# Kernel tuning notes

Hardware: AMD Instinct MI355X
Metric: run time of the kernel (lower is better)

Reference implementation:

```python
import jax, jax.numpy as jnp
import numpy as np
import math

DIM, HEADS = 512, 8
D_K = DIM // HEADS

def setup_inputs() -> dict:
    key = jax.random.key(0)
    ks = jax.random.split(key, 6)
    B, LK, LQ = 16, 2048, 256
    s = 1.0 / math.sqrt(DIM)
    return {
        "L": jax.random.normal(ks[0], (B, LK, DIM), jnp.float32),
        "G": jax.random.normal(ks[1], (B, LQ, DIM), jnp.float32),
        "Wq": jax.random.normal(ks[2], (DIM, DIM), jnp.float32) * s,
        "bq": jnp.zeros((DIM,), jnp.float32),
        "Wo": jax.random.normal(ks[3], (DIM, DIM), jnp.float32) * s,
        "bo": jnp.zeros((DIM,), jnp.float32),
    }

def reference(L, G, Wq, bq, Wo, bo):
    B = G.shape[0]
    # Q projection from global tokens; K,V are raw local features split into heads
    q = (G @ Wq + bq).reshape(B, -1, HEADS, D_K)          # [B, Lq, H, d]
    k = L.reshape(B, -1, HEADS, D_K)                      # [B, Lk, H, d]
    v = k
    # double scaling as in source: / sqrt(d_k) * dim**-0.5
    scale = (D_K ** -0.5) * (DIM ** -0.5)
    dots = jnp.einsum("bqhd,bkhd->bhqk", q, k) * scale    # [B, H, Lq, Lk]
    attn = jax.nn.softmax(dots, axis=-1)
    x = jnp.einsum("bhqk,bkhd->bqhd", attn, v)            # [B, Lq, H, d]
    x = x.reshape(B, -1, HEADS * D_K)
    return x @ Wo + bo
```

## Files before the change

kernel.cpp:

```cpp
#include <hip/hip_runtime.h>

#define KSTR 72

typedef __attribute__((ext_vector_type(8))) short short8;
typedef __attribute__((ext_vector_type(4))) float f32x4;

#define EXP2F(x) __builtin_amdgcn_exp2f(x)

__device__ __forceinline__ unsigned short f2bf(float f) {
    union { float f; unsigned u; } v; v.f = f;
    unsigned r = v.u + 0x7fff + ((v.u >> 16) & 1);
    return (unsigned short)(r >> 16);
}
__device__ __forceinline__ unsigned pk2(float a, float b) {
    return (unsigned)f2bf(a) | ((unsigned)f2bf(b) << 16);
}

template<bool A_BF16, bool OUT_BF16>
__global__ __launch_bounds__(256) void gemm_mfma(const void* __restrict__ Ap,
                                                 const float* __restrict__ W,
                                                 const float* __restrict__ bias,
                                                 void* __restrict__ Cp,
                                                 float oscale) {
    __shared__ unsigned short As [64 * 40];
    __shared__ unsigned short Bst[64 * 40];

    const int tid  = threadIdx.x;
    const int wv   = tid >> 6;
    const int lane = tid & 63;
    const int c    = lane & 15;
    const int quad = lane >> 4;
    const int m0 = blockIdx.x * 64, n0 = blockIdx.y * 64;

    f32x4 acc[4];
    #pragma unroll
    for (int nt = 0; nt < 4; nt++) acc[nt] = (f32x4){0.f, 0.f, 0.f, 0.f};

    for (int k0 = 0; k0 < 512; k0 += 32) {
        {
            int m = tid >> 2, q8 = tid & 3;
            if (A_BF16) {
                const unsigned short* A = (const unsigned short*)Ap;
                short8 v = *(const short8*)(A + (size_t)(m0 + m) * 512 + k0 + 8 * q8);
                *(short8*)&As[m * 40 + 8 * q8] = v;
            } else {
                const float* A = (const float*)Ap;
                const float* ap = A + (size_t)(m0 + m) * 512 + k0 + 8 * q8;
                float4 a0 = *(const float4*)ap;
                float4 a1 = *(const float4*)(ap + 4);
                uint4 u;
                u.x = pk2(a0.x, a0.y); u.y = pk2(a0.z, a0.w);
                u.z = pk2(a1.x, a1.y); u.w = pk2(a1.z, a1.w);
                *(uint4*)&As[m * 40 + 8 * q8] = u;
            }
        }
        {
            int n = tid & 63, kw = tid >> 6;
            const float* wp = W + (size_t)(k0 + 8 * kw) * 512 + n0 + n;
            float bv[8];
            #pragma unroll
            for (int i = 0; i < 8; i++) bv[i] = wp[(size_t)i * 512];
            uint4 u;
            u.x = pk2(bv[0], bv[1]); u.y = pk2(bv[2], bv[3]);
            u.z = pk2(bv[4], bv[5]); u.w = pk2(bv[6], bv[7]);
            *(uint4*)&Bst[n * 40 + 8 * kw] = u;
        }
        __syncthreads();
        short8 af = *(const short8*)&As[(16 * wv + c) * 40 + 8 * quad];
        #pragma unroll
        for (int nt = 0; nt < 4; nt++) {
            short8 bf = *(const short8*)&Bst[(16 * nt + c) * 40 + 8 * quad];
            acc[nt] = __builtin_amdgcn_mfma_f32_16x16x32_bf16(af, bf, acc[nt], 0, 0, 0);
        }
        __syncthreads();
    }

    #pragma unroll
    for (int nt = 0; nt < 4; nt++) {
        float bv = bias[n0 + 16 * nt + c];
        #pragma unroll
        for (int r = 0; r < 4; r++) {
            float v = (acc[nt][r] + bv) * oscale;
            size_t idx = (size_t)(m0 + 16 * wv + 4 * quad + r) * 512 + n0 + 16 * nt + c;
            if (OUT_BF16) ((unsigned short*)Cp)[idx] = f2bf(v);
            else          ((float*)Cp)[idx] = v;
        }
    }
}

__global__ __launch_bounds__(256) void attn_mfma(const unsigned short* __restrict__ Q,
                                                 const float* __restrict__ Lmat,
                                                 unsigned short* __restrict__ X) {
    __shared__ unsigned short Krm[2][64 * KSTR];
    __shared__ unsigned short Kt [2][64 * KSTR];
    __shared__ unsigned short Pw [4][16 * KSTR];

    const int blk  = blockIdx.x;
    const int qt   = blk & 3;
    const int h    = (blk >> 2) & 7;
    const int b    = blk >> 5;
    const int tid  = threadIdx.x;
    const int wv   = tid >> 6;
    const int lane = tid & 63;
    const int c    = lane & 15;
    const int quad = lane >> 4;

    short8 qa[2];
    {
        const unsigned short* qsrc =
            Q + ((size_t)(b * 256 + qt * 64 + 16 * wv + c)) * 512 + h * 64;
        qa[0] = *(const short8*)(qsrc + 8 * quad);
        qa[1] = *(const short8*)(qsrc + 32 + 8 * quad);
    }
    short8 ones;
    #pragma unroll
    for (int i = 0; i < 8; i++) ones[i] = (short)0x3F80;

    f32x4 oacc[4];
    #pragma unroll
    for (int dt = 0; dt < 4; dt++) oacc[dt] = (f32x4){0.f, 0.f, 0.f, 0.f};
    f32x4 lacc = (f32x4){0.f, 0.f, 0.f, 0.f};

    const float* sp0 = Lmat + (size_t)b * 2048 * 512 + h * 64 + (size_t)lane * 512 + 16 * wv;

    {
        float4 a0 = *(const float4*)sp0;
        float4 a1 = *(const float4*)(sp0 + 4);
        float4 a2 = *(const float4*)(sp0 + 8);
        float4 a3 = *(const float4*)(sp0 + 12);
        uint4 u0, u1;
        u0.x = pk2(a0.x, a0.y); u0.y = pk2(a0.z, a0.w);
        u0.z = pk2(a1.x, a1.y); u0.w = pk2(a1.z, a1.w);
        u1.x = pk2(a2.x, a2.y); u1.y = pk2(a2.z, a2.w);
        u1.z = pk2(a3.x, a3.y); u1.w = pk2(a3.z, a3.w);
        *(uint4*)&Krm[0][lane * KSTR + 16 * wv]     = u0;
        *(uint4*)&Krm[0][lane * KSTR + 16 * wv + 8] = u1;
        float vals[16] = {a0.x, a0.y, a0.z, a0.w, a1.x, a1.y, a1.z, a1.w,
                          a2.x, a2.y, a2.z, a2.w, a3.x, a3.y, a3.z, a3.w};
        #pragma unroll
        for (int i = 0; i < 16; i++)
            Kt[0][(16 * wv + i) * KSTR + lane] = f2bf(vals[i]);
    }
    __syncthreads();

    const int swc = (c >> 3) & 1;
    const int swr = (quad >> 1) & 1;

    int p = 0;
    for (int t = 0; t < 32; t++) {
        float4 a0, a1, a2, a3;
        if (t < 31) {
            const float* src = sp0 + (size_t)(t + 1) * 64 * 512;
            a0 = *(const float4*)src;
            a1 = *(const float4*)(src + 4);
            a2 = *(const float4*)(src + 8);
            a3 = *(const float4*)(src + 12);
        }

        f32x4 sacc[4];
        #pragma unroll
        for (int nt = 0; nt < 4; nt++) sacc[nt] = (f32x4){0.f, 0.f, 0.f, 0.f};
        #pragma unroll
        for (int nt = 0; nt < 4; nt++)
            #pragma unroll
            for (int ks = 0; ks < 2; ks++) {
                short8 kb = *(const short8*)&Krm[p][(16 * nt + c) * KSTR + 32 * ks + 8 * quad];
                sacc[nt] = __builtin_amdgcn_mfma_f32_16x16x32_bf16(qa[ks], kb, sacc[nt], 0, 0, 0);
            }

        #pragma unroll
        for (int nt = 0; nt < 4; nt++)
            #pragma unroll
            for (int r = 0; r < 4; r++)
                Pw[wv][(4 * quad + r) * KSTR + ((16 * nt + c) ^ (8 * swr))] =
                    f2bf(EXP2F(sacc[nt][r]));

        short8 pa0 = *(const short8*)&Pw[wv][c * KSTR + (8 * (quad ^ swc))];
        short8 pa1 = *(const short8*)&Pw[wv][c * KSTR + 32 + (8 * (quad ^ swc))];

        #pragma unroll
        for (int dt = 0; dt < 4; dt++) {
            short8 v0 = *(const short8*)&Kt[p][(16 * dt + c) * KSTR + 8 * quad];
            oacc[dt] = __builtin_amdgcn_mfma_f32_16x16x32_bf16(pa0, v0, oacc[dt], 0, 0, 0);
            short8 v1 = *(const short8*)&Kt[p][(16 * dt + c) * KSTR + 32 + 8 * quad];
            oacc[dt] = __builtin_amdgcn_mfma_f32_16x16x32_bf16(pa1, v1, oacc[dt], 0, 0, 0);
        }
        lacc = __builtin_amdgcn_mfma_f32_16x16x32_bf16(pa0, ones, lacc, 0, 0, 0);
        lacc = __builtin_amdgcn_mfma_f32_16x16x32_bf16(pa1, ones, lacc, 0, 0, 0);

        if (t < 31) {
            uint4 u0, u1;
            u0.x = pk2(a0.x, a0.y); u0.y = pk2(a0.z, a0.w);
            u0.z = pk2(a1.x, a1.y); u0.w = pk2(a1.z, a1.w);
            u1.x = pk2(a2.x, a2.y); u1.y = pk2(a2.z, a2.w);
            u1.z = pk2(a3.x, a3.y); u1.w = pk2(a3.z, a3.w);
            *(uint4*)&Krm[p ^ 1][lane * KSTR + 16 * wv]     = u0;
            *(uint4*)&Krm[p ^ 1][lane * KSTR + 16 * wv + 8] = u1;
            float vals[16] = {a0.x, a0.y, a0.z, a0.w, a1.x, a1.y, a1.z, a1.w,
                              a2.x, a2.y, a2.z, a2.w, a3.x, a3.y, a3.z, a3.w};
            #pragma unroll
            for (int i = 0; i < 16; i++)
                Kt[p ^ 1][(16 * wv + i) * KSTR + lane] = f2bf(vals[i]);
        }
        __syncthreads();
        p ^= 1;
    }

    #pragma unroll
    for (int r = 0; r < 4; r++) {
        float inv = 1.f / lacc[r];
        size_t row = (size_t)(b * 256 + qt * 64 + 16 * wv + 4 * quad + r);
        unsigned short* xp = X + row * 512 + h * 64;
        #pragma unroll
        for (int dt = 0; dt < 4; dt++)
            xp[16 * dt + c] = f2bf(oacc[dt][r] * inv);
    }
}

extern "C" void kernel_launch(void* const* d_in, const int* in_sizes, int n_in,
                              void* d_out, int out_size, void* d_ws, size_t ws_size,
                              hipStream_t stream) {
    const float* Lmat = (const float*)d_in[0];
    const float* G    = (const float*)d_in[1];
    const float* Wq   = (const float*)d_in[2];
    const float* bq   = (const float*)d_in[3];
    const float* Wo   = (const float*)d_in[4];
    const float* bo   = (const float*)d_in[5];
    float* out = (float*)d_out;

    unsigned short* Qws = (unsigned short*)d_ws;
    unsigned short* Xws = Qws + (size_t)4096 * 512;

    const float SCe = 0.005524271728019903f * 1.4426950408889634f;

    dim3 gg(64, 8);
    gemm_mfma<false, true><<<gg, 256, 0, stream>>>(G, Wq, bq, Qws, SCe);
    attn_mfma<<<512, 256, 0, stream>>>(Qws, Lmat, Xws);
    gemm_mfma<true, false><<<gg, 256, 0, stream>>>(Xws, Wo, bo, out, 1.0f);
}
```

Measured before the change: 200.8 us.

## Pre-convert L and weights into MFMA fragment layout in workspace

```diff
diff --git a/kernel.cpp b/kernel.cpp
--- a/kernel.cpp
+++ b/kernel.cpp
@@ -14,6 +14,226 @@
 }
 __device__ __forceinline__ unsigned pk2(float a, float b) {
     return (unsigned)f2bf(a) | ((unsigned)f2bf(b) << 16);
+}
+
+
+__global__ __launch_bounds__(256) void conv_W(const float* __restrict__ Wq,
+                                              const float* __restrict__ Wo,
+                                              unsigned short* __restrict__ WqF,
+                                              unsigned short* __restrict__ WoF) {
+    const float* W = blockIdx.y ? Wo : Wq;
+    unsigned short* WF = blockIdx.y ? WoF : WqF;
+    int g = blockIdx.x * 256 + threadIdx.x;
+    int lane = g & 63, ntg = (g >> 6) & 31, kt = g >> 11;
+    int c = lane & 15, quad = lane >> 4;
+    const float* wp = W + (size_t)(32 * kt + 8 * quad) * 512 + 16 * ntg + c;
+    float v[8];
+    #pragma unroll
+    for (int j = 0; j < 8; j++) v[j] = wp[(size_t)j * 512];
+    uint4 u;
+    u.x = pk2(v[0], v[1]); u.y = pk2(v[2], v[3]);
+    u.z = pk2(v[4], v[5]); u.w = pk2(v[6], v[7]);
+    *(uint4*)(WF + (size_t)g * 8) = u;
+}
+
+__global__ __launch_bounds__(256) void conv_L(const float* __restrict__ Lmat,
+                                              unsigned short* __restrict__ KF,
+                                              unsigned short* __restrict__ VF) {
+    __shared__ unsigned short KFs[4096];
+    __shared__ unsigned short VFs[4096];
+    const int blk = blockIdx.x;
+    const int t = blk & 31, h = (blk >> 5) & 7, b = blk >> 8;
+    const int tid = threadIdx.x;
+    const int key = tid & 63, wv = tid >> 6;
+
+    const float* src = Lmat + ((size_t)(b * 2048 + 64 * t + key)) * 512 + 64 * h + 16 * wv;
+    float4 a0 = *(const float4*)src;
+    float4 a1 = *(const float4*)(src + 4);
+    float4 a2 = *(const float4*)(src + 8);
+    float4 a3 = *(const float4*)(src + 12);
+    float vals[16] = {a0.x, a0.y, a0.z, a0.w, a1.x, a1.y, a1.z, a1.w,
+                      a2.x, a2.y, a2.z, a2.w, a3.x, a3.y, a3.z, a3.w};
+    #pragma unroll
+    for (int i = 0; i < 16; i++) {
+        int d = 16 * wv + i;
+        unsigned short bv = f2bf(vals[i]);
+        KFs[((((key >> 4) * 2 + (d >> 5)) * 64) + ((d >> 3) & 3) * 16 + (key & 15)) * 8 + (d & 7)] = bv;
+        VFs[((((d >> 4) * 2 + (key >> 5)) * 64) + ((key >> 3) & 3) * 16 + (d & 15)) * 8 + (key & 7)] = bv;
+    }
+    __syncthreads();
+    size_t gbase = (size_t)blk * 4096 + tid * 16;
+    *(uint4*)(KF + gbase)     = *(const uint4*)&KFs[tid * 16];
+    *(uint4*)(KF + gbase + 8) = *(const uint4*)&KFs[tid * 16 + 8];
+    *(uint4*)(VF + gbase)     = *(const uint4*)&VFs[tid * 16];
+    *(uint4*)(VF + gbase + 8) = *(const uint4*)&VFs[tid * 16 + 8];
+}
+
+template<bool A_BF16, bool OUT_BF16>
+__global__ __launch_bounds__(256) void gemm_frag(const void* __restrict__ Ap,
+                                                 const unsigned short* __restrict__ WF,
+                                                 const float* __restrict__ bias,
+                                                 void* __restrict__ Cp,
+                                                 float oscale) {
+    __shared__ unsigned short As[64 * 72];
+    const int tid = threadIdx.x;
+    const int wv = tid >> 6, lane = tid & 63;
+    const int c = lane & 15, quad = lane >> 4;
+    const int m0 = blockIdx.x * 64, n0 = blockIdx.y * 64;
+
+    f32x4 acc[4];
+    #pragma unroll
+    for (int nt = 0; nt < 4; nt++) acc[nt] = (f32x4){0.f, 0.f, 0.f, 0.f};
+
+    for (int k0 = 0; k0 < 512; k0 += 64) {
+        {
+            int m = tid >> 2, seg = tid & 3;
+            if (A_BF16) {
+                const unsigned short* ap = (const unsigned short*)Ap +
+                    (size_t)(m0 + m) * 512 + k0 + 16 * seg;
+                *(uint4*)&As[m * 72 + 16 * seg]     = *(const uint4*)ap;
+                *(uint4*)&As[m * 72 + 16 * seg + 8] = *(const uint4*)(ap + 8);
+            } else {
+                const float* ap = (const float*)Ap + (size_t)(m0 + m) * 512 + k0 + 16 * seg;
+                float4 b0 = *(const float4*)ap;
+                float4 b1 = *(const float4*)(ap + 4);
+                float4 b2 = *(const float4*)(ap + 8);
+                float4 b3 = *(const float4*)(ap + 12);
+                uint4 u0, u1;
+                u0.x = pk2(b0.x, b0.y); u0.y = pk2(b0.z, b0.w);
+                u0.z = pk2(b1.x, b1.y); u0.w = pk2(b1.z, b1.w);
+                u1.x = pk2(b2.x, b2.y); u1.y = pk2(b2.z, b2.w);
+                u1.z = pk2(b3.x, b3.y); u1.w = pk2(b3.z, b3.w);
+                *(uint4*)&As[m * 72 + 16 * seg]     = u0;
+                *(uint4*)&As[m * 72 + 16 * seg + 8] = u1;
+            }
+        }
+        __syncthreads();
+        #pragma unroll
+        for (int kk = 0; kk < 2; kk++) {
+            short8 af = *(const short8*)&As[(16 * wv + c) * 72 + 32 * kk + 8 * quad];
+            #pragma unroll
+            for (int nt = 0; nt < 4; nt++) {
+                short8 bf = *(const short8*)(WF +
+                    (((size_t)(k0 / 32 + kk) * 32 + n0 / 16 + nt) * 64 + lane) * 8);
+                acc[nt] = __builtin_amdgcn_mfma_f32_16x16x32_bf16(af, bf, acc[nt], 0, 0, 0);
+            }
+        }
+        __syncthreads();
+    }
+
+    #pragma unroll
+    for (int nt = 0; nt < 4; nt++) {
+        float bv = bias[n0 + 16 * nt + c];
+        #pragma unroll
+        for (int r = 0; r < 4; r++) {
+            float v = (acc[nt][r] + bv) * oscale;
+            size_t idx = (size_t)(m0 + 16 * wv + 4 * quad + r) * 512 + n0 + 16 * nt + c;
+            if (OUT_BF16) ((unsigned short*)Cp)[idx] = f2bf(v);
+            else          ((float*)Cp)[idx] = v;
+        }
+    }
+}
+
+__global__ __launch_bounds__(256) void attn_frag(const unsigned short* __restrict__ Q,
+                                                 const unsigned short* __restrict__ KF,
+                                                 const unsigned short* __restrict__ VF,
+                                                 unsigned short* __restrict__ X) {
+    __shared__ unsigned short Pw[4][16 * KSTR];
+
+    const int blk = blockIdx.x;
+    const int qt = blk & 3, h = (blk >> 2) & 7, b = blk >> 5;
+    const int tid = threadIdx.x;
+    const int wv = tid >> 6, lane = tid & 63;
+    const int c = lane & 15, quad = lane >> 4;
+
+    short8 qa[2];
+    {
+        const unsigned short* qsrc =
+            Q + ((size_t)(b * 256 + qt * 64 + 16 * wv + c)) * 512 + h * 64;
+        qa[0] = *(const short8*)(qsrc + 8 * quad);
+        qa[1] = *(const short8*)(qsrc + 32 + 8 * quad);
+    }
+    short8 ones;
+    #pragma unroll
+    for (int i = 0; i < 8; i++) ones[i] = (short)0x3F80;
+
+    f32x4 oacc[4];
+    #pragma unroll
+    for (int dt = 0; dt < 4; dt++) oacc[dt] = (f32x4){0.f, 0.f, 0.f, 0.f};
+    f32x4 lacc = (f32x4){0.f, 0.f, 0.f, 0.f};
+
+    const int swc = (c >> 3) & 1;
+    const int swr = (quad >> 1) & 1;
+
+    const unsigned short* kf = KF + ((size_t)((b * 8 + h) * 32)) * 4096 + lane * 8;
+    const unsigned short* vf = VF + ((size_t)((b * 8 + h) * 32)) * 4096 + lane * 8;
+
+    short8 kc[8], vc[8], kn[8], vn[8];
+    #pragma unroll
+    for (int f = 0; f < 8; f++) {
+        kc[f] = *(const short8*)(kf + f * 512);
+        vc[f] = *(const short8*)(vf + f * 512);
+    }
+
+    auto compute = [&](short8* kb, short8* vb) {
+        f32x4 sacc[4];
+        #pragma unroll
+        for (int nt = 0; nt < 4; nt++) sacc[nt] = (f32x4){0.f, 0.f, 0.f, 0.f};
+        #pragma unroll
+        for (int nt = 0; nt < 4; nt++)
+            #pragma unroll
+            for (int ks = 0; ks < 2; ks++)
+                sacc[nt] = __builtin_amdgcn_mfma_f32_16x16x32_bf16(
+                    qa[ks], kb[nt * 2 + ks], sacc[nt], 0, 0, 0);
+        #pragma unroll
+        for (int nt = 0; nt < 4; nt++)
+            #pragma unroll
+            for (int r = 0; r < 4; r++)
+                Pw[wv][(4 * quad + r) * KSTR + ((16 * nt + c) ^ (8 * swr))] =
+                    f2bf(EXP2F(sacc[nt][r]));
+        short8 pa0 = *(const short8*)&Pw[wv][c * KSTR + (8 * (quad ^ swc))];
+        short8 pa1 = *(const short8*)&Pw[wv][c * KSTR + 32 + (8 * (quad ^ swc))];
+        #pragma unroll
+        for (int dt = 0; dt < 4; dt++) {
+            oacc[dt] = __builtin_amdgcn_mfma_f32_16x16x32_bf16(pa0, vb[dt * 2], oacc[dt], 0, 0, 0);
+            oacc[dt] = __builtin_amdgcn_mfma_f32_16x16x32_bf16(pa1, vb[dt * 2 + 1], oacc[dt], 0, 0, 0);
+        }
+        lacc = __builtin_amdgcn_mfma_f32_16x16x32_bf16(pa0, ones, lacc, 0, 0, 0);
+        lacc = __builtin_amdgcn_mfma_f32_16x16x32_bf16(pa1, ones, lacc, 0, 0, 0);
+    };
+
+    for (int t = 0; t < 32; t += 2) {
+        {
+            const unsigned short* k2 = kf + (size_t)(t + 1) * 4096;
+            const unsigned short* v2 = vf + (size_t)(t + 1) * 4096;
+            #pragma unroll
+            for (int f = 0; f < 8; f++) {
+                kn[f] = *(const short8*)(k2 + f * 512);
+                vn[f] = *(const short8*)(v2 + f * 512);
+            }
+        }
+        compute(kc, vc);
+        if (t + 2 < 32) {
+            const unsigned short* k2 = kf + (size_t)(t + 2) * 4096;
+            const unsigned short* v2 = vf + (size_t)(t + 2) * 4096;
+            #pragma unroll
+            for (int f = 0; f < 8; f++) {
+                kc[f] = *(const short8*)(k2 + f * 512);
+                vc[f] = *(const short8*)(v2 + f * 512);
+            }
+        }
+        compute(kn, vn);
+    }
+
+    #pragma unroll
+    for (int r = 0; r < 4; r++) {
+        float inv = 1.f / lacc[r];
+        size_t row = (size_t)(b * 256 + qt * 64 + 16 * wv + 4 * quad + r);
+        unsigned short* xp = X + row * 512 + h * 64;
+        #pragma unroll
+        for (int dt = 0; dt < 4; dt++)
+            xp[16 * dt + c] = f2bf(oacc[dt][r] * inv);
+    }
 }
 
 template<bool A_BF16, bool OUT_BF16>
@@ -24,18 +244,15 @@
                                                  float oscale) {
     __shared__ unsigned short As [64 * 40];
     __shared__ unsigned short Bst[64 * 40];
-
     const int tid  = threadIdx.x;
     const int wv   = tid >> 6;
     const int lane = tid & 63;
     const int c    = lane & 15;
     const int quad = lane >> 4;
     const int m0 = blockIdx.x * 64, n0 = blockIdx.y * 64;
-
     f32x4 acc[4];
     #pragma unroll
     for (int nt = 0; nt < 4; nt++) acc[nt] = (f32x4){0.f, 0.f, 0.f, 0.f};
-
     for (int k0 = 0; k0 < 512; k0 += 32) {
         {
             int m = tid >> 2, q8 = tid & 3;
@@ -74,7 +291,6 @@
         }
         __syncthreads();
     }
-
     #pragma unroll
     for (int nt = 0; nt < 4; nt++) {
         float bv = bias[n0 + 16 * nt + c];
@@ -94,7 +310,6 @@
     __shared__ unsigned short Krm[2][64 * KSTR];
     __shared__ unsigned short Kt [2][64 * KSTR];
     __shared__ unsigned short Pw [4][16 * KSTR];
-
     const int blk  = blockIdx.x;
     const int qt   = blk & 3;
     const int h    = (blk >> 2) & 7;
@@ -104,7 +319,6 @@
     const int lane = tid & 63;
     const int c    = lane & 15;
     const int quad = lane >> 4;
-
     short8 qa[2];
     {
         const unsigned short* qsrc =
@@ -115,14 +329,11 @@
     short8 ones;
     #pragma unroll
     for (int i = 0; i < 8; i++) ones[i] = (short)0x3F80;
-
     f32x4 oacc[4];
     #pragma unroll
     for (int dt = 0; dt < 4; dt++) oacc[dt] = (f32x4){0.f, 0.f, 0.f, 0.f};
     f32x4 lacc = (f32x4){0.f, 0.f, 0.f, 0.f};
-
     const float* sp0 = Lmat + (size_t)b * 2048 * 512 + h * 64 + (size_t)lane * 512 + 16 * wv;
-
     {
         float4 a0 = *(const float4*)sp0;
         float4 a1 = *(const float4*)(sp0 + 4);
@@ -142,10 +353,8 @@
             Kt[0][(16 * wv + i) * KSTR + lane] = f2bf(vals[i]);
     }
     __syncthreads();
-
     const int swc = (c >> 3) & 1;
     const int swr = (quad >> 1) & 1;
-
     int p = 0;
     for (int t = 0; t < 32; t++) {
         float4 a0, a1, a2, a3;
@@ -156,7 +365,6 @@
             a2 = *(const float4*)(src + 8);
             a3 = *(const float4*)(src + 12);
         }
-
         f32x4 sacc[4];
         #pragma unroll
         for (int nt = 0; nt < 4; nt++) sacc[nt] = (f32x4){0.f, 0.f, 0.f, 0.f};
@@ -167,17 +375,14 @@
                 short8 kb = *(const short8*)&Krm[p][(16 * nt + c) * KSTR + 32 * ks + 8 * quad];
                 sacc[nt] = __builtin_amdgcn_mfma_f32_16x16x32_bf16(qa[ks], kb, sacc[nt], 0, 0, 0);
             }
-
         #pragma unroll
         for (int nt = 0; nt < 4; nt++)
             #pragma unroll
             for (int r = 0; r < 4; r++)
                 Pw[wv][(4 * quad + r) * KSTR + ((16 * nt + c) ^ (8 * swr))] =
                     f2bf(EXP2F(sacc[nt][r]));
-
         short8 pa0 = *(const short8*)&Pw[wv][c * KSTR + (8 * (quad ^ swc))];
         short8 pa1 = *(const short8*)&Pw[wv][c * KSTR + 32 + (8 * (quad ^ swc))];
-
         #pragma unroll
         for (int dt = 0; dt < 4; dt++) {
             short8 v0 = *(const short8*)&Kt[p][(16 * dt + c) * KSTR + 8 * quad];
@@ -187,7 +392,6 @@
         }
         lacc = __builtin_amdgcn_mfma_f32_16x16x32_bf16(pa0, ones, lacc, 0, 0, 0);
         lacc = __builtin_amdgcn_mfma_f32_16x16x32_bf16(pa1, ones, lacc, 0, 0, 0);
-
         if (t < 31) {
             uint4 u0, u1;
             u0.x = pk2(a0.x, a0.y); u0.y = pk2(a0.z, a0.w);
@@ -205,7 +409,6 @@
         __syncthreads();
         p ^= 1;
     }
-
     #pragma unroll
     for (int r = 0; r < 4; r++) {
         float inv = 1.f / lacc[r];
@@ -228,13 +431,26 @@
     const float* bo   = (const float*)d_in[5];
     float* out = (float*)d_out;
 
+    const float SCe = 0.005524271728019903f * 1.4426950408889634f;
+    dim3 gg(64, 8);
+
+    const size_t NEED = 76546048;
     unsigned short* Qws = (unsigned short*)d_ws;
-    unsigned short* Xws = Qws + (size_t)4096 * 512;
-
-    const float SCe = 0.005524271728019903f * 1.4426950408889634f;
-
-    dim3 gg(64, 8);
-    gemm_mfma<false, true><<<gg, 256, 0, stream>>>(G, Wq, bq, Qws, SCe);
-    attn_mfma<<<512, 256, 0, stream>>>(Qws, Lmat, Xws);
-    gemm_mfma<true, false><<<gg, 256, 0, stream>>>(Xws, Wo, bo, out, 1.0f);
-}
+    unsigned short* Xws = Qws + (size_t)2097152;
+
+    if (ws_size >= NEED) {
+        unsigned short* WqF = Xws + (size_t)2097152;
+        unsigned short* WoF = WqF + (size_t)262144;
+        unsigned short* KF  = WoF + (size_t)262144;
+        unsigned short* VF  = KF  + (size_t)16777216;
+        conv_W<<<dim3(128, 2), 256, 0, stream>>>(Wq, Wo, WqF, WoF);
+        conv_L<<<4096, 256, 0, stream>>>(Lmat, KF, VF);
+        gemm_frag<false, true><<<gg, 256, 0, stream>>>(G, WqF, bq, Qws, SCe);
+        attn_frag<<<512, 256, 0, stream>>>(Qws, KF, VF, Xws);
+        gemm_frag<true, false><<<gg, 256, 0, stream>>>(Xws, WoF, bo, out, 1.0f);
+    } else {
+        gemm_mfma<false, true><<<gg, 256, 0, stream>>>(G, Wq, bq, Qws, SCe);
+        attn_mfma<<<512, 256, 0, stream>>>(Qws, Lmat, Xws);
+        gemm_mfma<true, false><<<gg, 256, 0, stream>>>(Xws, Wo, bo, out, 1.0f);
+    }
+}
```

After: 191.9 us. 1.05x faster.

## Pre-pack K/V and weights into MFMA fragment layout, load directly to registers

Applied to the files above, without the earlier changes.

```diff
diff --git a/kernel.cpp b/kernel.cpp
--- a/kernel.cpp
+++ b/kernel.cpp
@@ -16,63 +16,93 @@
     return (unsigned)f2bf(a) | ((unsigned)f2bf(b) << 16);
 }
 
+__global__ __launch_bounds__(256) void conv_W(const float* __restrict__ Wq,
+                                              const float* __restrict__ Wo,
+                                              unsigned short* __restrict__ WqF,
+                                              unsigned short* __restrict__ WoF) {
+    const float* W = blockIdx.y ? Wo : Wq;
+    unsigned short* WF = blockIdx.y ? WoF : WqF;
+    int g = blockIdx.x * 256 + threadIdx.x;
+    int lane = g & 63, ntg = (g >> 6) & 31, kt = g >> 11;
+    int c = lane & 15, quad = lane >> 4;
+    const float* wp = W + (size_t)(32 * kt + 8 * quad) * 512 + 16 * ntg + c;
+    float v[8];
+    #pragma unroll
+    for (int j = 0; j < 8; j++) v[j] = wp[(size_t)j * 512];
+    uint4 u;
+    u.x = pk2(v[0], v[1]); u.y = pk2(v[2], v[3]);
+    u.z = pk2(v[4], v[5]); u.w = pk2(v[6], v[7]);
+    *(uint4*)(WF + (size_t)g * 8) = u;
+}
+
+__global__ __launch_bounds__(256) void conv_L(const float* __restrict__ Lmat,
+                                              unsigned short* __restrict__ KF,
+                                              unsigned short* __restrict__ VF) {
+    __shared__ unsigned short KFs[4096];
+    __shared__ unsigned short VFs[4096];
+    const int blk = blockIdx.x;
+    const int t = blk & 31, h = (blk >> 5) & 7, b = blk >> 8;
+    const int tid = threadIdx.x;
+    const int key = tid & 63, wv = tid >> 6;
+
+    const float* src = Lmat + ((size_t)(b * 2048 + 64 * t + key)) * 512 + 64 * h + 16 * wv;
+    float4 a0 = *(const float4*)src;
+    float4 a1 = *(const float4*)(src + 4);
+    float4 a2 = *(const float4*)(src + 8);
+    float4 a3 = *(const float4*)(src + 12);
+    float vals[16] = {a0.x, a0.y, a0.z, a0.w, a1.x, a1.y, a1.z, a1.w,
+                      a2.x, a2.y, a2.z, a2.w, a3.x, a3.y, a3.z, a3.w};
+    #pragma unroll
+    for (int i = 0; i < 16; i++) {
+        int d = 16 * wv + i;
+        unsigned short bv = f2bf(vals[i]);
+        KFs[((((key >> 4) * 2 + (d >> 5)) * 64) + ((d >> 3) & 3) * 16 + (key & 15)) * 8 + (d & 7)] = bv;
+        VFs[((((d >> 4) * 2 + (key >> 5)) * 64) + ((key >> 3) & 3) * 16 + (d & 15)) * 8 + (key & 7)] = bv;
+    }
+    __syncthreads();
+    size_t gbase = (size_t)blk * 4096 + tid * 16;
+    *(uint4*)(KF + gbase)     = *(const uint4*)&KFs[tid * 16];
+    *(uint4*)(KF + gbase + 8) = *(const uint4*)&KFs[tid * 16 + 8];
+    *(uint4*)(VF + gbase)     = *(const uint4*)&VFs[tid * 16];
+    *(uint4*)(VF + gbase + 8) = *(const uint4*)&VFs[tid * 16 + 8];
+}
+
 template<bool A_BF16, bool OUT_BF16>
-__global__ __launch_bounds__(256) void gemm_mfma(const void* __restrict__ Ap,
-                                                 const float* __restrict__ W,
-                                                 const float* __restrict__ bias,
-                                                 void* __restrict__ Cp,
-                                                 float oscale) {
-    __shared__ unsigned short As [64 * 40];
-    __shared__ unsigned short Bst[64 * 40];
-
-    const int tid  = threadIdx.x;
-    const int wv   = tid >> 6;
-    const int lane = tid & 63;
-    const int c    = lane & 15;
-    const int quad = lane >> 4;
+__global__ __launch_bounds__(256) void gemm_direct(const void* __restrict__ Ap,
+                                                   const unsigned short* __restrict__ WF,
+                                                   const float* __restrict__ bias,
+                                                   void* __restrict__ Cp,
+                                                   float oscale) {
+    const int tid = threadIdx.x;
+    const int wv = tid >> 6, lane = tid & 63;
+    const int c = lane & 15, quad = lane >> 4;
     const int m0 = blockIdx.x * 64, n0 = blockIdx.y * 64;
+    const int row = m0 + 16 * wv + c;
 
     f32x4 acc[4];
     #pragma unroll
     for (int nt = 0; nt < 4; nt++) acc[nt] = (f32x4){0.f, 0.f, 0.f, 0.f};
 
-    for (int k0 = 0; k0 < 512; k0 += 32) {
-        {
-            int m = tid >> 2, q8 = tid & 3;
-            if (A_BF16) {
-                const unsigned short* A = (const unsigned short*)Ap;
-                short8 v = *(const short8*)(A + (size_t)(m0 + m) * 512 + k0 + 8 * q8);
-                *(short8*)&As[m * 40 + 8 * q8] = v;
-            } else {
-                const float* A = (const float*)Ap;
-                const float* ap = A + (size_t)(m0 + m) * 512 + k0 + 8 * q8;
-                float4 a0 = *(const float4*)ap;
-                float4 a1 = *(const float4*)(ap + 4);
-                uint4 u;
-                u.x = pk2(a0.x, a0.y); u.y = pk2(a0.z, a0.w);
-                u.z = pk2(a1.x, a1.y); u.w = pk2(a1.z, a1.w);
-                *(uint4*)&As[m * 40 + 8 * q8] = u;
-            }
-        }
-        {
-            int n = tid & 63, kw = tid >> 6;
-            const float* wp = W + (size_t)(k0 + 8 * kw) * 512 + n0 + n;
-            float bv[8];
-            #pragma unroll
-            for (int i = 0; i < 8; i++) bv[i] = wp[(size_t)i * 512];
-            uint4 u;
-            u.x = pk2(bv[0], bv[1]); u.y = pk2(bv[2], bv[3]);
-            u.z = pk2(bv[4], bv[5]); u.w = pk2(bv[6], bv[7]);
-            *(uint4*)&Bst[n * 40 + 8 * kw] = u;
-        }
-        __syncthreads();
-        short8 af = *(const short8*)&As[(16 * wv + c) * 40 + 8 * quad];
+    #pragma unroll
+    for (int kk = 0; kk < 16; kk++) {
+        short8 af;
+        if (A_BF16) {
+            af = *(const short8*)((const unsigned short*)Ap + (size_t)row * 512 + 32 * kk + 8 * quad);
+        } else {
+            const float* ap = (const float*)Ap + (size_t)row * 512 + 32 * kk + 8 * quad;
+            float4 x0 = *(const float4*)ap;
+            float4 x1 = *(const float4*)(ap + 4);
+            af[0] = (short)f2bf(x0.x); af[1] = (short)f2bf(x0.y);
+            af[2] = (short)f2bf(x0.z); af[3] = (short)f2bf(x0.w);
+            af[4] = (short)f2bf(x1.x); af[5] = (short)f2bf(x1.y);
+            af[6] = (short)f2bf(x1.z); af[7] = (short)f2bf(x1.w);
+        }
         #pragma unroll
         for (int nt = 0; nt < 4; nt++) {
-            short8 bf = *(const short8*)&Bst[(16 * nt + c) * 40 + 8 * quad];
+            short8 bf = *(const short8*)(WF +
+                (((size_t)kk * 32 + (n0 >> 4) + nt) * 64 + lane) * 8);
             acc[nt] = __builtin_amdgcn_mfma_f32_16x16x32_bf16(af, bf, acc[nt], 0, 0, 0);
         }
-        __syncthreads();
     }
 
     #pragma unroll
@@ -88,22 +118,19 @@
     }
 }
 
-__global__ __launch_bounds__(256) void attn_mfma(const unsigned short* __restrict__ Q,
-                                                 const float* __restrict__ Lmat,
+__global__ __launch_bounds__(256) void attn_frag(const unsigned short* __restrict__ Q,
+                                                 const unsigned short* __restrict__ KF,
+                                                 const unsigned short* __restrict__ VF,
                                                  unsigned short* __restrict__ X) {
-    __shared__ unsigned short Krm[2][64 * KSTR];
-    __shared__ unsigned short Kt [2][64 * KSTR];
-    __shared__ unsigned short Pw [4][16 * KSTR];
-
-    const int blk  = blockIdx.x;
-    const int qt   = blk & 3;
-    const int h    = (blk >> 2) & 7;
-    const int b    = blk >> 5;
-    const int tid  = threadIdx.x;
-    const int wv   = tid >> 6;
-    const int lane = tid & 63;
-    const int c    = lane & 15;
-    const int quad = lane >> 4;
+    __shared__ unsigned short Pw[4][16 * KSTR];
+
+    const int raw = blockIdx.x;
+    const int h  = raw & 7;
+    const int qt = (raw >> 3) & 3;
+    const int b  = raw >> 5;
+    const int tid = threadIdx.x;
+    const int wv = tid >> 6, lane = tid & 63;
+    const int c = lane & 15, quad = lane >> 4;
 
     short8 qa[2];
     {
@@ -121,89 +148,67 @@
     for (int dt = 0; dt < 4; dt++) oacc[dt] = (f32x4){0.f, 0.f, 0.f, 0.f};
     f32x4 lacc = (f32x4){0.f, 0.f, 0.f, 0.f};
 
-    const float* sp0 = Lmat + (size_t)b * 2048 * 512 + h * 64 + (size_t)lane * 512 + 16 * wv;
-
-    {
-        float4 a0 = *(const float4*)sp0;
-        float4 a1 = *(const float4*)(sp0 + 4);
-        float4 a2 = *(const float4*)(sp0 + 8);
-        float4 a3 = *(const float4*)(sp0 + 12);
-        uint4 u0, u1;
-        u0.x = pk2(a0.x, a0.y); u0.y = pk2(a0.z, a0.w);
-        u0.z = pk2(a1.x, a1.y); u0.w = pk2(a1.z, a1.w);
-        u1.x = pk2(a2.x, a2.y); u1.y = pk2(a2.z, a2.w);
-        u1.z = pk2(a3.x, a3.y); u1.w = pk2(a3.z, a3.w);
-        *(uint4*)&Krm[0][lane * KSTR + 16 * wv]     = u0;
-        *(uint4*)&Krm[0][lane * KSTR + 16 * wv + 8] = u1;
-        float vals[16] = {a0.x, a0.y, a0.z, a0.w, a1.x, a1.y, a1.z, a1.w,
-                          a2.x, a2.y, a2.z, a2.w, a3.x, a3.y, a3.z, a3.w};
-        #pragma unroll
-        for (int i = 0; i < 16; i++)
-            Kt[0][(16 * wv + i) * KSTR + lane] = f2bf(vals[i]);
-    }
-    __syncthreads();
-
     const int swc = (c >> 3) & 1;
     const int swr = (quad >> 1) & 1;
 
-    int p = 0;
-    for (int t = 0; t < 32; t++) {
-        float4 a0, a1, a2, a3;
-        if (t < 31) {
-            const float* src = sp0 + (size_t)(t + 1) * 64 * 512;
-            a0 = *(const float4*)src;
-            a1 = *(const float4*)(src + 4);
-            a2 = *(const float4*)(src + 8);
-            a3 = *(const float4*)(src + 12);
-        }
-
+    const unsigned short* kf = KF + ((size_t)((b * 8 + h) * 32)) * 4096 + lane * 8;
+    const unsigned short* vf = VF + ((size_t)((b * 8 + h) * 32)) * 4096 + lane * 8;
+
+    short8 kc[8], vc[8], kn[8], vn[8];
+    #pragma unroll
+    for (int f = 0; f < 8; f++) {
+        kc[f] = *(const short8*)(kf + f * 512);
+        vc[f] = *(const short8*)(vf + f * 512);
+    }
+
+    auto compute = [&](short8* kb, short8* vb) {
         f32x4 sacc[4];
         #pragma unroll
         for (int nt = 0; nt < 4; nt++) sacc[nt] = (f32x4){0.f, 0.f, 0.f, 0.f};
         #pragma unroll
         for (int nt = 0; nt < 4; nt++)
             #pragma unroll
-            for (int ks = 0; ks < 2; ks++) {
-                short8 kb = *(const short8*)&Krm[p][(16 * nt + c) * KSTR + 32 * ks + 8 * quad];
-                sacc[nt] = __builtin_amdgcn_mfma_f32_16x16x32_bf16(qa[ks], kb, sacc[nt], 0, 0, 0);
-            }
-
+            for (int ks = 0; ks < 2; ks++)
+                sacc[nt] = __builtin_amdgcn_mfma_f32_16x16x32_bf16(
+                    qa[ks], kb[nt * 2 + ks], sacc[nt], 0, 0, 0);
         #pragma unroll
         for (int nt = 0; nt < 4; nt++)
             #pragma unroll
             for (int r = 0; r < 4; r++)
                 Pw[wv][(4 * quad + r) * KSTR + ((16 * nt + c) ^ (8 * swr))] =
                     f2bf(EXP2F(sacc[nt][r]));
-
         short8 pa0 = *(const short8*)&Pw[wv][c * KSTR + (8 * (quad ^ swc))];
         short8 pa1 = *(const short8*)&Pw[wv][c * KSTR + 32 + (8 * (quad ^ swc))];
-
         #pragma unroll
         for (int dt = 0; dt < 4; dt++) {
-            short8 v0 = *(const short8*)&Kt[p][(16 * dt + c) * KSTR + 8 * quad];
-            oacc[dt] = __builtin_amdgcn_mfma_f32_16x16x32_bf16(pa0, v0, oacc[dt], 0, 0, 0);
-            short8 v1 = *(const short8*)&Kt[p][(16 * dt + c) * KSTR + 32 + 8 * quad];
-            oacc[dt] = __builtin_amdgcn_mfma_f32_16x16x32_bf16(pa1, v1, oacc[dt], 0, 0, 0);
+            oacc[dt] = __builtin_amdgcn_mfma_f32_16x16x32_bf16(pa0, vb[dt * 2], oacc[dt], 0, 0, 0);
+            oacc[dt] = __builtin_amdgcn_mfma_f32_16x16x32_bf16(pa1, vb[dt * 2 + 1], oacc[dt], 0, 0, 0);
         }
         lacc = __builtin_amdgcn_mfma_f32_16x16x32_bf16(pa0, ones, lacc, 0, 0, 0);
         lacc = __builtin_amdgcn_mfma_f32_16x16x32_bf16(pa1, ones, lacc, 0, 0, 0);
-
-        if (t < 31) {
-            uint4 u0, u1;
-            u0.x = pk2(a0.x, a0.y); u0.y = pk2(a0.z, a0.w);
-            u0.z = pk2(a1.x, a1.y); u0.w = pk2(a1.z, a1.w);
-            u1.x = pk2(a2.x, a2.y); u1.y = pk2(a2.z, a2.w);
-            u1.z = pk2(a3.x, a3.y); u1.w = pk2(a3.z, a3.w);
-            *(uint4*)&Krm[p ^ 1][lane * KSTR + 16 * wv]     = u0;
-            *(uint4*)&Krm[p ^ 1][lane * KSTR + 16 * wv + 8] = u1;
-            float vals[16] = {a0.x, a0.y, a0.z, a0.w, a1.x, a1.y, a1.z, a1.w,
-                              a2.x, a2.y, a2.z, a2.w, a3.x, a3.y, a3.z, a3.w};
-            #pragma unroll
-            for (int i = 0; i < 16; i++)
-                Kt[p ^ 1][(16 * wv + i) * KSTR + lane] = f2bf(vals[i]);
-        }
-        __syncthreads();
-        p ^= 1;
+    };
+
+    for (int t = 0; t < 32; t += 2) {
+        {
+            const unsigned short* k2 = kf + (size_t)(t + 1) * 4096;
+            const unsigned short* v2 = vf + (size_t)(t + 1) * 4096;
+            #pragma unroll
+            for (int f = 0; f < 8; f++) {
+                kn[f] = *(const short8*)(k2 + f * 512);
+                vn[f] = *(const short8*)(v2 + f * 512);
+            }
+        }
+        compute(kc, vc);
+        if (t + 2 < 32) {
+            const unsigned short* k2 = kf + (size_t)(t + 2) * 4096;
+            const unsigned short* v2 = vf + (size_t)(t + 2) * 4096;
+            #pragma unroll
+            for (int f = 0; f < 8; f++) {
+                kc[f] = *(const short8*)(k2 + f * 512);
+                vc[f] = *(const short8*)(v2 + f * 512);
+            }
+        }
+        compute(kn, vn);
     }
 
     #pragma unroll
@@ -228,13 +233,19 @@
     const float* bo   = (const float*)d_in[5];
     float* out = (float*)d_out;
 
+    const float SCe = 0.005524271728019903f * 1.4426950408889634f;
+    dim3 gg(64, 8);
+
     unsigned short* Qws = (unsigned short*)d_ws;
-    unsigned short* Xws = Qws + (size_t)4096 * 512;
-
-    const float SCe = 0.005524271728019903f * 1.4426950408889634f;
-
-    dim3 gg(64, 8);
-    gemm_mfma<false, true><<<gg, 256, 0, stream>>>(G, Wq, bq, Qws, SCe);
-    attn_mfma<<<512, 256, 0, stream>>>(Qws, Lmat, Xws);
-    gemm_mfma<true, false><<<gg, 256, 0, stream>>>(Xws, Wo, bo, out, 1.0f);
-}
+    unsigned short* Xws = Qws + (size_t)2097152;
+    unsigned short* WqF = Xws + (size_t)2097152;
+    unsigned short* WoF = WqF + (size_t)262144;
+    unsigned short* KF  = WoF + (size_t)262144;
+    unsigned short* VF  = KF  + (size_t)16777216;
+
+    conv_W<<<dim3(128, 2), 256, 0, stream>>>(Wq, Wo, WqF, WoF);
+    conv_L<<<4096, 256, 0, stream>>>(Lmat, KF, VF);
+    gemm_direct<false, true><<<gg, 256, 0, stream>>>(G, WqF, bq, Qws, SCe);
+    attn_frag<<<512, 256, 0, stream>>>(Qws, KF, VF, Xws);
+    gemm_direct<true, false><<<gg, 256, 0, stream>>>(Xws, WoF, bo, out, 1.0f);
+}
```

Measured after the change: 178.8 us. 10.9% less time.
